# Optimization experiments

Hardware: AMD Instinct MI355X
Metric: run time of the kernel (lower is better)

Reference implementation:

```python
import jax, jax.numpy as jnp
import numpy as np

N, IN_DIM, OUT_DIM, BASIS = 262144, 128, 256, 7

def setup_inputs() -> dict:
    key = jax.random.key(0)
    k1, k2, k3, k4, k5 = jax.random.split(key, 5)
    return {
        "x": jax.random.normal(k1, (N, IN_DIM), dtype=jnp.float32),
        "W_s": jax.random.normal(k2, (IN_DIM, BASIS), dtype=jnp.float32) * (1.0 / np.sqrt(IN_DIM)),
        "b_s": jax.random.normal(k3, (BASIS,), dtype=jnp.float32) * 0.01,
        "W_m": jax.random.normal(k4, (2 * BASIS, 1), dtype=jnp.float32) * (1.0 / np.sqrt(2 * BASIS)),
        "b_m": jax.random.normal(k5, (1,), dtype=jnp.float32) * 0.01,
    }

def reference(x, W_s, b_s, W_m, b_m):
    # Fmap: linear -> [sin, cos] -> linear(->1)
    h = x @ W_s + b_s                                  # [N, basis]
    feats = jnp.concatenate((jnp.sin(h), jnp.cos(h)), axis=-1)  # [N, 2*basis]
    y = feats @ W_m + b_m                              # [N, 1]
    # Original uses `[Fmap(...)] * out_dim`: the SAME module repeated, so all
    # out_dim output columns are identical -> tile the single column.
    return jnp.broadcast_to(y, (y.shape[0], OUT_DIM))  # [N, out_dim]
```

## Files before the change

kernel.cpp:

```cpp
#include <hip/hip_runtime.h>

#define N_ROWS  262144
#define IN_DIM  128
#define OUT_DIM 256
#define BASIS   7

#define GRID    2048
#define BLOCK   256
#define NWAVES  ((GRID * BLOCK) / 64)
#define ITERS   (N_ROWS / (NWAVES * 4))

__global__ __launch_bounds__(BLOCK) void flinear_kernel(
    const float* __restrict__ x,
    const float* __restrict__ W_s,
    const float* __restrict__ b_s,
    const float* __restrict__ W_m,
    const float* __restrict__ b_m,
    float* __restrict__ out)
{
    const int tid  = blockIdx.x * blockDim.x + threadIdx.x;
    const int wave = tid >> 6;
    const int lane = threadIdx.x & 63;
    const int sub  = lane & 15;
    const int grp  = lane >> 4;

    float w0[4][BASIS], w1[4][BASIS];
    #pragma unroll
    for (int e = 0; e < 4; ++e) {
        #pragma unroll
        for (int j = 0; j < BASIS; ++j) {
            w0[e][j] = W_s[(sub * 4 + e) * BASIS + j];
            w1[e][j] = W_s[(64 + sub * 4 + e) * BASIS + j];
        }
    }
    float bs[BASIS], wm_s[BASIS], wm_c[BASIS];
    #pragma unroll
    for (int j = 0; j < BASIS; ++j) {
        bs[j]   = b_s[j];
        wm_s[j] = W_m[j];
        wm_c[j] = W_m[BASIS + j];
    }
    const float bm = b_m[0];

    const int rowStride = NWAVES * 4;

    int row = wave * 4 + grp;
    const float* xp = x + row * IN_DIM + sub * 4;

    float4 xa = *reinterpret_cast<const float4*>(xp);
    float4 xb = *reinterpret_cast<const float4*>(xp + 64);

    #pragma unroll
    for (int i = 0; i < ITERS; ++i) {
        float4 na = xa, nb = xb;
        if (i + 1 < ITERS) {
            const float* np = xp + rowStride * IN_DIM;
            na = *reinterpret_cast<const float4*>(np);
            nb = *reinterpret_cast<const float4*>(np + 64);
        }

        float h[BASIS];
        #pragma unroll
        for (int j = 0; j < BASIS; ++j) {
            h[j] = xa.x * w0[0][j] + xa.y * w0[1][j] + xa.z * w0[2][j] + xa.w * w0[3][j]
                 + xb.x * w1[0][j] + xb.y * w1[1][j] + xb.z * w1[2][j] + xb.w * w1[3][j];
        }

        #pragma unroll
        for (int m = 1; m < 16; m <<= 1) {
            #pragma unroll
            for (int j = 0; j < BASIS; ++j)
                h[j] += __shfl_xor(h[j], m, 64);
        }

        float y = bm;
        #pragma unroll
        for (int j = 0; j < BASIS; ++j) {
            float s, c;
            __sincosf(h[j] + bs[j], &s, &c);
            y += s * wm_s[j] + c * wm_c[j];
        }

        const float4 v = make_float4(y, y, y, y);
        float* o = out + row * OUT_DIM + sub * 4;
        *reinterpret_cast<float4*>(o)       = v;
        *reinterpret_cast<float4*>(o + 64)  = v;
        *reinterpret_cast<float4*>(o + 128) = v;
        *reinterpret_cast<float4*>(o + 192) = v;

        xp  += rowStride * IN_DIM;
        row += rowStride;
        xa = na; xb = nb;
    }
}

extern "C" void kernel_launch(void* const* d_in, const int* in_sizes, int n_in,
                              void* d_out, int out_size, void* d_ws, size_t ws_size,
                              hipStream_t stream) {
    const float* x   = (const float*)d_in[0];
    const float* W_s = (const float*)d_in[1];
    const float* b_s = (const float*)d_in[2];
    const float* W_m = (const float*)d_in[3];
    const float* b_m = (const float*)d_in[4];
    float* out = (float*)d_out;

    flinear_kernel<<<GRID, BLOCK, 0, stream>>>(x, W_s, b_s, W_m, b_m, out);
}
```

Before: 79.90 us.

## Split into compute-y and separate broadcast-store kernels via workspace

Splits the fused kernel in two. The first kernel computes one scalar per row and writes it to a workspace buffer. The second kernel streams the broadcast output with fully coalesced, grid-strided float4 stores. The aim is to separate the read-heavy phase from the write-heavy phase so that each kernel has a simpler memory access pattern. The cost is an extra kernel launch and a small workspace round trip, and a fused fallback path is kept for when there is no workspace.

```diff
diff --git a/kernel.cpp b/kernel.cpp
--- a/kernel.cpp
+++ b/kernel.cpp
@@ -10,13 +10,13 @@
 #define NWAVES  ((GRID * BLOCK) / 64)
 #define ITERS   (N_ROWS / (NWAVES * 4))
 
-__global__ __launch_bounds__(BLOCK) void flinear_kernel(
+__global__ __launch_bounds__(BLOCK) void compute_y_kernel(
     const float* __restrict__ x,
     const float* __restrict__ W_s,
     const float* __restrict__ b_s,
     const float* __restrict__ W_m,
     const float* __restrict__ b_m,
-    float* __restrict__ out)
+    float* __restrict__ y_out)
 {
     const int tid  = blockIdx.x * blockDim.x + threadIdx.x;
     const int wave = tid >> 6;
@@ -43,7 +43,6 @@
     const float bm = b_m[0];
 
     const int rowStride = NWAVES * 4;
-
     int row = wave * 4 + grp;
     const float* xp = x + row * IN_DIM + sub * 4;
 
@@ -81,16 +80,87 @@
             y += s * wm_s[j] + c * wm_c[j];
         }
 
+        if (sub == 0) y_out[row] = y;
+
+        xp  += rowStride * IN_DIM;
+        row += rowStride;
+        xa = na; xb = nb;
+    }
+}
+
+#define NQUADS (N_ROWS * (OUT_DIM / 4))
+__global__ __launch_bounds__(BLOCK) void broadcast_kernel(
+    const float* __restrict__ y,
+    float4* __restrict__ out4)
+{
+    const int tid    = blockIdx.x * blockDim.x + threadIdx.x;
+    const int stride = GRID * BLOCK;
+
+    int idx = tid;
+    float v = y[idx >> 6];
+    #pragma unroll 4
+    for (int k = 0; k < NQUADS / stride - 1; ++k) {
+        float nv = y[(idx + stride) >> 6];
+        out4[idx] = make_float4(v, v, v, v);
+        idx += stride;
+        v = nv;
+    }
+    out4[idx] = make_float4(v, v, v, v);
+}
+
+__global__ __launch_bounds__(BLOCK) void fused_kernel(
+    const float* __restrict__ x, const float* __restrict__ W_s,
+    const float* __restrict__ b_s, const float* __restrict__ W_m,
+    const float* __restrict__ b_m, float* __restrict__ out)
+{
+    const int tid  = blockIdx.x * blockDim.x + threadIdx.x;
+    const int wave = tid >> 6;
+    const int lane = threadIdx.x & 63;
+    const int sub  = lane & 15;
+    const int grp  = lane >> 4;
+
+    float w0[4][BASIS], w1[4][BASIS];
+    #pragma unroll
+    for (int e = 0; e < 4; ++e)
+        #pragma unroll
+        for (int j = 0; j < BASIS; ++j) {
+            w0[e][j] = W_s[(sub * 4 + e) * BASIS + j];
+            w1[e][j] = W_s[(64 + sub * 4 + e) * BASIS + j];
+        }
+    float bs[BASIS], wm_s[BASIS], wm_c[BASIS];
+    #pragma unroll
+    for (int j = 0; j < BASIS; ++j) {
+        bs[j] = b_s[j]; wm_s[j] = W_m[j]; wm_c[j] = W_m[BASIS + j];
+    }
+    const float bm = b_m[0];
+
+    for (int rowBase = wave * 4; rowBase < N_ROWS; rowBase += NWAVES * 4) {
+        const int row = rowBase + grp;
+        const float4 xa = *reinterpret_cast<const float4*>(x + row * IN_DIM + sub * 4);
+        const float4 xb = *reinterpret_cast<const float4*>(x + row * IN_DIM + 64 + sub * 4);
+        float h[BASIS];
+        #pragma unroll
+        for (int j = 0; j < BASIS; ++j)
+            h[j] = xa.x * w0[0][j] + xa.y * w0[1][j] + xa.z * w0[2][j] + xa.w * w0[3][j]
+                 + xb.x * w1[0][j] + xb.y * w1[1][j] + xb.z * w1[2][j] + xb.w * w1[3][j];
+        #pragma unroll
+        for (int m = 1; m < 16; m <<= 1)
+            #pragma unroll
+            for (int j = 0; j < BASIS; ++j)
+                h[j] += __shfl_xor(h[j], m, 64);
+        float y = bm;
+        #pragma unroll
+        for (int j = 0; j < BASIS; ++j) {
+            float s, c;
+            __sincosf(h[j] + bs[j], &s, &c);
+            y += s * wm_s[j] + c * wm_c[j];
+        }
         const float4 v = make_float4(y, y, y, y);
         float* o = out + row * OUT_DIM + sub * 4;
         *reinterpret_cast<float4*>(o)       = v;
         *reinterpret_cast<float4*>(o + 64)  = v;
         *reinterpret_cast<float4*>(o + 128) = v;
         *reinterpret_cast<float4*>(o + 192) = v;
-
-        xp  += rowStride * IN_DIM;
-        row += rowStride;
-        xa = na; xb = nb;
     }
 }
 
@@ -104,5 +174,11 @@
     const float* b_m = (const float*)d_in[4];
     float* out = (float*)d_out;
 
-    flinear_kernel<<<GRID, BLOCK, 0, stream>>>(x, W_s, b_s, W_m, b_m, out);
+    if (ws_size >= (size_t)N_ROWS * sizeof(float)) {
+        float* y = (float*)d_ws;
+        compute_y_kernel<<<GRID, BLOCK, 0, stream>>>(x, W_s, b_s, W_m, b_m, y);
+        broadcast_kernel<<<GRID, BLOCK, 0, stream>>>(y, (float4*)out);
+    } else {
+        fused_kernel<<<GRID, BLOCK, 0, stream>>>(x, W_s, b_s, W_m, b_m, out);
+    }
 }
```

New measurement: 97.79 us. +22.4%, slower.
